# Kernel optimization log

Hardware: AMD Instinct MI355X
Metric: run time of the kernel (lower is better)

## Reference

```python
import jax, jax.numpy as jnp
import numpy as np

TEMPERATURE = 0.5

def setup_inputs() -> dict:
    key = jax.random.key(0)
    k1, k2 = jax.random.split(key)
    B, D = 4096, 256
    return {
        "first_transformed": jax.random.normal(k1, (B, D), dtype=jnp.float32),
        "second_transformed": jax.random.normal(k2, (B, D), dtype=jnp.float32),
    }

def reference(first_transformed, second_transformed):
    B = first_transformed.shape[0]
    z = jnp.concatenate([first_transformed, second_transformed], axis=0)  # [2B, D]
    z = z / jnp.linalg.norm(z, axis=1, keepdims=True)
    sim = jnp.matmul(z, z.T) / TEMPERATURE  # [2B, 2B]
    n = 2 * B
    # exclude self-similarity from the denominator (mask diagonal)
    diag_mask = jnp.eye(n, dtype=bool)
    denom = jax.nn.logsumexp(jnp.where(diag_mask, -jnp.inf, sim), axis=1)  # [2B]
    # positive pair for row i is row (i+B) mod 2B
    pos_idx = (jnp.arange(n) + B) % n
    pos = sim[jnp.arange(n), pos_idx]  # [2B]
    # loss = 1/(2B) * sum_i (-log(exp(pos_i)/denom_i)) = mean(denom - pos)
    return jnp.mean(denom - pos)
```

## Files before the change

kernel.cpp:

```cpp
#include <hip/hip_runtime.h>
#include <hip/hip_bf16.h>
#include <math.h>


#define NROWS 8192
#define BHALF 4096
#define DDIM  256
#define ROWB  512
#define JT    64
#define TILEB (JT * ROWB)
#define NSLOT 35
#define SSTRIDE 40

#define SQRT_K1 1.6986436f
#define LN2F 0.6931471805599453f

typedef __attribute__((ext_vector_type(8))) __bf16 bf16x8;
typedef __attribute__((ext_vector_type(4))) float f32x4;

#if __has_builtin(__builtin_amdgcn_exp2f)
#define FEXP2(x) __builtin_amdgcn_exp2f(x)
#else
#define FEXP2(x) __exp2f(x)
#endif
#if __has_builtin(__builtin_amdgcn_logf)
#define FLOG2(x) __builtin_amdgcn_logf(x)
#else
#define FLOG2(x) __log2f(x)
#endif

__device__ __forceinline__ float bfu(unsigned short u) {
  union { unsigned v; float f; } x; x.v = ((unsigned)u) << 16; return x.f;
}

__global__ __launch_bounds__(256) void norm_kernel(
    const float* __restrict__ a, const float* __restrict__ b,
    char* __restrict__ zb, float* __restrict__ selfdot) {
  int row = blockIdx.x * 4 + (threadIdx.x >> 6);
  int lane = threadIdx.x & 63;
  const float* src = (row < BHALF) ? (a + (size_t)row * DDIM)
                                   : (b + (size_t)(row - BHALF) * DDIM);
  float4 v = ((const float4*)src)[lane];
  float ss = v.x * v.x + v.y * v.y + v.z * v.z + v.w * v.w;
  #pragma unroll
  for (int m = 1; m < 64; m <<= 1) ss += __shfl_xor(ss, m, 64);
  float inv = rsqrtf(ss);
  inv = inv * (1.5f - 0.5f * ss * inv * inv);
  float sc = inv * SQRT_K1;

  union { __hip_bfloat16 h; unsigned short u; } c0, c1, c2, c3;
  c0.h = __float2bfloat16(v.x * sc);
  c1.h = __float2bfloat16(v.y * sc);
  c2.h = __float2bfloat16(v.z * sc);
  c3.h = __float2bfloat16(v.w * sc);
  float q0 = bfu(c0.u), q1 = bfu(c1.u), q2 = bfu(c2.u), q3 = bfu(c3.u);
  float sq = q0 * q0 + q1 * q1 + q2 * q2 + q3 * q3;
  #pragma unroll
  for (int m = 1; m < 64; m <<= 1) sq += __shfl_xor(sq, m, 64);

  ushort4 o = make_ushort4(c0.u, c1.u, c2.u, c3.u);
  int off = row * ROWB + ((lane * 8) ^ ((row & 7) << 4));
  *(ushort4*)(zb + off) = o;
  if (lane == 0) selfdot[row] = sq;
}

__global__ __launch_bounds__(256, 2) void sim_kernel(
    const char* __restrict__ zb, float* __restrict__ s_part) {
  __shared__ __align__(16) char lds[2 * TILEB];
  __shared__ float cred[2][4][64];

  int bid = blockIdx.x;
  bool heavy = (bid < 128);
  int t  = heavy ? (bid & 31) : ((bid - 128) & 31);
  int gg = heavy ? (bid >> 5) : (4 + ((bid - 128) >> 5));
  int NJT = heavy ? 5 : 4;
  int ustrip = (t + gg) & 31;
  int u16 = (t + 16) & 31;

  int wave = threadIdx.x >> 6;
  int lane = threadIdx.x & 63;
  int lrow = lane & 15;
  int kgrp = lane >> 4;
  int r0 = t * 256 + wave * 64;

  bf16x8 af[4][8];
  {
    int sw = (lrow & 7) << 4;
    #pragma unroll
    for (int rf = 0; rf < 4; ++rf) {
      const char* rp = zb + (size_t)(r0 + rf * 16 + lrow) * ROWB;
      #pragma unroll
      for (int kk = 0; kk < 8; ++kk)
        af[rf][kk] = *(const bf16x8*)(rp + ((kk * 64 + kgrp * 16) ^ sw));
    }
  }

  float sacc[4][4] = {};
  float cacc[4] = {};
  f32x4 C0, C1, C2, C3;
  bf16x8 bfv[8];

  #define STAGE_SLOT(dstbuf, j0, kkh) do {                                    \
    const char* g_ = zb +                                                     \
        (size_t)((j0) + wave * 16 + lrow) * ROWB +                            \
        (((kkh) * 64 + kgrp * 16) ^ ((lane & 7) << 4));                       \
    char* l_ = lds + (dstbuf) * TILEB + (wave * 8 + (kkh)) * 1024;            \
    __builtin_amdgcn_global_load_lds(                                         \
        (const __attribute__((address_space(1))) void*)g_,                    \
        (__attribute__((address_space(3))) void*)l_, 16, 0, 0);               \
  } while (0)

  #define DSREAD(bufi, ct) do {                                               \
    const char* lbr = lds + (bufi) * TILEB + lane * 16;                       \
    _Pragma("unroll")                                                         \
    for (int kk = 0; kk < 8; ++kk)                                            \
      bfv[kk] = *(const bf16x8*)(lbr + ((ct) * 8 + kk) * 1024);               \
  } while (0)

  #define MFMA32() do {                                                       \
    C0 = (f32x4){0.f, 0.f, 0.f, 0.f};                                         \
    C1 = (f32x4){0.f, 0.f, 0.f, 0.f};                                         \
    C2 = (f32x4){0.f, 0.f, 0.f, 0.f};                                         \
    C3 = (f32x4){0.f, 0.f, 0.f, 0.f};                                         \
    __builtin_amdgcn_s_setprio(1);                                            \
    _Pragma("unroll")                                                         \
    for (int kk = 0; kk < 8; ++kk) {                                          \
      C0 = __builtin_amdgcn_mfma_f32_16x16x32_bf16(af[0][kk], bfv[kk], C0, 0, 0, 0); \
      C1 = __builtin_amdgcn_mfma_f32_16x16x32_bf16(af[1][kk], bfv[kk], C1, 0, 0, 0); \
      C2 = __builtin_amdgcn_mfma_f32_16x16x32_bf16(af[2][kk], bfv[kk], C2, 0, 0, 0); \
      C3 = __builtin_amdgcn_mfma_f32_16x16x32_bf16(af[3][kk], bfv[kk], C3, 0, 0, 0); \
    }                                                                         \
    __builtin_amdgcn_s_setprio(0);                                            \
  } while (0)

  #define FLUSHC(ct) do {                                                     \
    float cs = 0.f;                                                           \
    _Pragma("unroll")                                                         \
    for (int r = 0; r < 4; ++r) {                                             \
      float e0 = FEXP2(C0[r]), e1 = FEXP2(C1[r]);                             \
      float e2 = FEXP2(C2[r]), e3 = FEXP2(C3[r]);                             \
      sacc[0][r] += e0; sacc[1][r] += e1;                                     \
      sacc[2][r] += e2; sacc[3][r] += e3;                                     \
      cs += (e0 + e1) + (e2 + e3);                                            \
    }                                                                         \
    cacc[ct] += cs;                                                           \
  } while (0)

  #pragma unroll
  for (int kk = 0; kk < 8; ++kk) STAGE_SLOT(0, ustrip * 256, kk);
  asm volatile("s_waitcnt vmcnt(0)" ::: "memory");
  __builtin_amdgcn_sched_barrier(0);
  __builtin_amdgcn_s_barrier();

  for (int jt = 0; jt < NJT; ++jt) {
    int nb = jt & 1;
    bool last = (jt == NJT - 1);
    int nj = jt + 1;
    int nextbase = (nj < 4) ? (ustrip * 256 + nj * 64) : (u16 * 256 + gg * 64);

    #pragma unroll
    for (int ct = 0; ct < 4; ++ct) {
      DSREAD(nb, ct);
      if (!last) {
        STAGE_SLOT(nb ^ 1, nextbase, 2 * ct);
        STAGE_SLOT(nb ^ 1, nextbase, 2 * ct + 1);
      }
      MFMA32();
      FLUSHC(ct);
    }

    bool harvest = (jt < 4) && (gg > 0);
    if (harvest) {
      #pragma unroll
      for (int c2 = 0; c2 < 4; ++c2) {
        float v = cacc[c2];
        v += __shfl_xor(v, 16, 64);
        v += __shfl_xor(v, 32, 64);
        if (kgrp == 0) cred[jt & 1][wave][c2 * 16 + lrow] = v;
      }
    }
    #pragma unroll
    for (int c2 = 0; c2 < 4; ++c2) cacc[c2] = 0.f;

    if (jt == 3 || jt == 4) {
      int slot = (jt == 3) ? gg : 16 + gg;
      #pragma unroll
      for (int rf = 0; rf < 4; ++rf) {
        #pragma unroll
        for (int r = 0; r < 4; ++r) {
          float v = sacc[rf][r];
          #pragma unroll
          for (int m = 1; m < 16; m <<= 1) v += __shfl_xor(v, m, 64);
          if (lrow == 0) {
            int grow = r0 + rf * 16 + kgrp * 4 + r;
            s_part[(size_t)grow * SSTRIDE + slot] = v;
          }
          sacc[rf][r] = 0.f;
        }
      }
    }

    asm volatile("s_waitcnt vmcnt(0)" ::: "memory");
    __builtin_amdgcn_sched_barrier(0);
    __builtin_amdgcn_s_barrier();

    if (harvest && wave == (jt & 3)) {
      int colrow = ustrip * 256 + jt * 64 + lane;
      float v = cred[jt & 1][0][lane] + cred[jt & 1][1][lane] +
                cred[jt & 1][2][lane] + cred[jt & 1][3][lane];
      s_part[(size_t)colrow * SSTRIDE + 19 + gg] = v;
    }
  }
  #undef FLUSHC
  #undef MFMA32
  #undef DSREAD
  #undef STAGE_SLOT
}

__global__ __launch_bounds__(256) void rowterm_kernel(
    const char* __restrict__ zb, const float* __restrict__ s_part,
    const float* __restrict__ selfdot, float* __restrict__ bpart) {
  int wave = threadIdx.x >> 6;
  int lane = threadIdx.x & 63;
  int rbase = blockIdx.x * 16 + wave * 4;
  float wacc = 0.f;
  #pragma unroll
  for (int rr = 0; rr < 4; ++rr) {
    int i = rbase + rr;
    int j = i ^ BHALF;
    int wo = (lane * 8) ^ ((i & 7) << 4);
    ushort4 zi = *(const ushort4*)(zb + (size_t)i * ROWB + wo);
    ushort4 zj = *(const ushort4*)(zb + (size_t)j * ROWB + wo);
    float dot = bfu(zi.x) * bfu(zj.x) + bfu(zi.y) * bfu(zj.y) +
                bfu(zi.z) * bfu(zj.z) + bfu(zi.w) * bfu(zj.w);
    float sp = (lane < NSLOT) ? s_part[(size_t)i * SSTRIDE + lane] : 0.f;
    #pragma unroll
    for (int m = 1; m < 64; m <<= 1) {
      dot += __shfl_xor(dot, m, 64);
      sp += __shfl_xor(sp, m, 64);
    }
    float S = sp - FEXP2(selfdot[i]);
    wacc += LN2F * (FLOG2(S) - dot);
  }
  __shared__ float red[4];
  if (lane == 0) red[wave] = wacc;
  __syncthreads();
  if (threadIdx.x == 0)
    bpart[blockIdx.x] = red[0] + red[1] + red[2] + red[3];
}

__global__ __launch_bounds__(512) void final_kernel(
    const float* __restrict__ bpart, float* __restrict__ out) {
  int t = threadIdx.x;
  float v = bpart[t];
  #pragma unroll
  for (int m = 1; m < 64; m <<= 1) v += __shfl_xor(v, m, 64);
  __shared__ float r2[8];
  if ((t & 63) == 0) r2[t >> 6] = v;
  __syncthreads();
  if (t == 0) {
    float s = 0.f;
    #pragma unroll
    for (int w = 0; w < 8; ++w) s += r2[w];
    out[0] = s / (float)NROWS;
  }
}

extern "C" void kernel_launch(void* const* d_in, const int* in_sizes, int n_in,
                              void* d_out, int out_size, void* d_ws, size_t ws_size,
                              hipStream_t stream) {
  const float* a = (const float*)d_in[0];
  const float* b = (const float*)d_in[1];
  float* out = (float*)d_out;
  char* ws = (char*)d_ws;

  char* zb = ws;
  float* selfdot = (float*)(ws + (size_t)NROWS * ROWB);
  float* s_part = selfdot + NROWS;
  float* bpart = s_part + (size_t)NROWS * SSTRIDE;

  hipLaunchKernelGGL(norm_kernel, dim3(NROWS / 4), dim3(256), 0, stream,
                     a, b, zb, selfdot);
  hipLaunchKernelGGL(sim_kernel, dim3(512), dim3(256), 0, stream,
                     zb, s_part);
  hipLaunchKernelGGL(rowterm_kernel, dim3(512), dim3(256), 0, stream,
                     zb, s_part, selfdot, bpart);
  hipLaunchKernelGGL(final_kernel, dim3(1), dim3(512), 0, stream, bpart, out);
}
```

Before: 43.59 us.

## Software-pipeline MFMA and exp flush with double accumulator sets

```diff
diff --git a/kernel.cpp b/kernel.cpp
--- a/kernel.cpp
+++ b/kernel.cpp
@@ -97,7 +97,8 @@
 
   float sacc[4][4] = {};
   float cacc[4] = {};
-  f32x4 C0, C1, C2, C3;
+  f32x4 X0, X1, X2, X3, Y0, Y1, Y2, Y3;
+  Y0 = Y1 = Y2 = Y3 = (f32x4){-1e30f, -1e30f, -1e30f, -1e30f};
   bf16x8 bfv[8];
 
   #define STAGE_SLOT(dstbuf, j0, kkh) do {                                    \
@@ -117,33 +118,61 @@
       bfv[kk] = *(const bf16x8*)(lbr + ((ct) * 8 + kk) * 1024);               \
   } while (0)
 
-  #define MFMA32() do {                                                       \
-    C0 = (f32x4){0.f, 0.f, 0.f, 0.f};                                         \
-    C1 = (f32x4){0.f, 0.f, 0.f, 0.f};                                         \
-    C2 = (f32x4){0.f, 0.f, 0.f, 0.f};                                         \
-    C3 = (f32x4){0.f, 0.f, 0.f, 0.f};                                         \
+  #define MFMA32(D0, D1, D2, D3) do {                                         \
+    D0 = (f32x4){0.f, 0.f, 0.f, 0.f};                                         \
+    D1 = (f32x4){0.f, 0.f, 0.f, 0.f};                                         \
+    D2 = (f32x4){0.f, 0.f, 0.f, 0.f};                                         \
+    D3 = (f32x4){0.f, 0.f, 0.f, 0.f};                                         \
     __builtin_amdgcn_s_setprio(1);                                            \
     _Pragma("unroll")                                                         \
     for (int kk = 0; kk < 8; ++kk) {                                          \
-      C0 = __builtin_amdgcn_mfma_f32_16x16x32_bf16(af[0][kk], bfv[kk], C0, 0, 0, 0); \
-      C1 = __builtin_amdgcn_mfma_f32_16x16x32_bf16(af[1][kk], bfv[kk], C1, 0, 0, 0); \
-      C2 = __builtin_amdgcn_mfma_f32_16x16x32_bf16(af[2][kk], bfv[kk], C2, 0, 0, 0); \
-      C3 = __builtin_amdgcn_mfma_f32_16x16x32_bf16(af[3][kk], bfv[kk], C3, 0, 0, 0); \
+      D0 = __builtin_amdgcn_mfma_f32_16x16x32_bf16(af[0][kk], bfv[kk], D0, 0, 0, 0); \
+      D1 = __builtin_amdgcn_mfma_f32_16x16x32_bf16(af[1][kk], bfv[kk], D1, 0, 0, 0); \
+      D2 = __builtin_amdgcn_mfma_f32_16x16x32_bf16(af[2][kk], bfv[kk], D2, 0, 0, 0); \
+      D3 = __builtin_amdgcn_mfma_f32_16x16x32_bf16(af[3][kk], bfv[kk], D3, 0, 0, 0); \
     }                                                                         \
     __builtin_amdgcn_s_setprio(0);                                            \
   } while (0)
 
-  #define FLUSHC(ct) do {                                                     \
+  #define FLUSHP(P0, P1, P2, P3, CIX) do {                                    \
     float cs = 0.f;                                                           \
     _Pragma("unroll")                                                         \
     for (int r = 0; r < 4; ++r) {                                             \
-      float e0 = FEXP2(C0[r]), e1 = FEXP2(C1[r]);                             \
-      float e2 = FEXP2(C2[r]), e3 = FEXP2(C3[r]);                             \
+      float e0 = FEXP2(P0[r]), e1 = FEXP2(P1[r]);                             \
+      float e2 = FEXP2(P2[r]), e3 = FEXP2(P3[r]);                             \
       sacc[0][r] += e0; sacc[1][r] += e1;                                     \
       sacc[2][r] += e2; sacc[3][r] += e3;                                     \
       cs += (e0 + e1) + (e2 + e3);                                            \
     }                                                                         \
-    cacc[ct] += cs;                                                           \
+    cacc[CIX] += cs;                                                          \
+  } while (0)
+
+  #define HARVEST(pj) do {                                                    \
+    _Pragma("unroll")                                                         \
+    for (int c2 = 0; c2 < 4; ++c2) {                                          \
+      float v = cacc[c2];                                                     \
+      v += __shfl_xor(v, 16, 64);                                             \
+      v += __shfl_xor(v, 32, 64);                                             \
+      if (kgrp == 0) cred[(pj) & 1][wave][c2 * 16 + lrow] = v;                \
+      cacc[c2] = 0.f;                                                         \
+    }                                                                         \
+  } while (0)
+
+  #define ROWFLUSH(slot) do {                                                 \
+    _Pragma("unroll")                                                         \
+    for (int rf = 0; rf < 4; ++rf) {                                          \
+      _Pragma("unroll")                                                       \
+      for (int r = 0; r < 4; ++r) {                                           \
+        float v = sacc[rf][r];                                                \
+        _Pragma("unroll")                                                     \
+        for (int m = 1; m < 16; m <<= 1) v += __shfl_xor(v, m, 64);           \
+        if (lrow == 0) {                                                      \
+          int grow = r0 + rf * 16 + kgrp * 4 + r;                             \
+          s_part[(size_t)grow * SSTRIDE + (slot)] = v;                        \
+        }                                                                     \
+        sacc[rf][r] = 0.f;                                                    \
+      }                                                                       \
+    }                                                                         \
   } while (0)
 
   #pragma unroll
@@ -153,65 +182,74 @@
   __builtin_amdgcn_s_barrier();
 
   for (int jt = 0; jt < NJT; ++jt) {
-    int nb = jt & 1;
+    int buf = jt & 1;
     bool last = (jt == NJT - 1);
     int nj = jt + 1;
     int nextbase = (nj < 4) ? (ustrip * 256 + nj * 64) : (u16 * 256 + gg * 64);
 
-    #pragma unroll
-    for (int ct = 0; ct < 4; ++ct) {
-      DSREAD(nb, ct);
-      if (!last) {
-        STAGE_SLOT(nb ^ 1, nextbase, 2 * ct);
-        STAGE_SLOT(nb ^ 1, nextbase, 2 * ct + 1);
-      }
-      MFMA32();
-      FLUSHC(ct);
-    }
-
-    bool harvest = (jt < 4) && (gg > 0);
-    if (harvest) {
-      #pragma unroll
-      for (int c2 = 0; c2 < 4; ++c2) {
-        float v = cacc[c2];
-        v += __shfl_xor(v, 16, 64);
-        v += __shfl_xor(v, 32, 64);
-        if (kgrp == 0) cred[jt & 1][wave][c2 * 16 + lrow] = v;
-      }
-    }
-    #pragma unroll
-    for (int c2 = 0; c2 < 4; ++c2) cacc[c2] = 0.f;
-
-    if (jt == 3 || jt == 4) {
-      int slot = (jt == 3) ? gg : 16 + gg;
-      #pragma unroll
-      for (int rf = 0; rf < 4; ++rf) {
-        #pragma unroll
-        for (int r = 0; r < 4; ++r) {
-          float v = sacc[rf][r];
-          #pragma unroll
-          for (int m = 1; m < 16; m <<= 1) v += __shfl_xor(v, m, 64);
-          if (lrow == 0) {
-            int grow = r0 + rf * 16 + kgrp * 4 + r;
-            s_part[(size_t)grow * SSTRIDE + slot] = v;
-          }
-          sacc[rf][r] = 0.f;
-        }
-      }
-    }
-
-    asm volatile("s_waitcnt vmcnt(0)" ::: "memory");
+    DSREAD(buf, 0);
+    if (!last) {
+      STAGE_SLOT(buf ^ 1, nextbase, 0);
+      STAGE_SLOT(buf ^ 1, nextbase, 1);
+      STAGE_SLOT(buf ^ 1, nextbase, 2);
+    }
+    FLUSHP(Y0, Y1, Y2, Y3, 3);
+    if (jt > 0) {
+      if (gg > 0) HARVEST(jt - 1);
+      else { cacc[0] = cacc[1] = cacc[2] = cacc[3] = 0.f; }
+      if (jt == 4) ROWFLUSH(gg);
+    }
+    MFMA32(X0, X1, X2, X3);
+    DSREAD(buf, 1);
+    if (!last) {
+      STAGE_SLOT(buf ^ 1, nextbase, 3);
+      STAGE_SLOT(buf ^ 1, nextbase, 4);
+      STAGE_SLOT(buf ^ 1, nextbase, 5);
+    }
+    FLUSHP(X0, X1, X2, X3, 0);
+    MFMA32(Y0, Y1, Y2, Y3);
+    DSREAD(buf, 2);
+    if (!last) {
+      STAGE_SLOT(buf ^ 1, nextbase, 6);
+      STAGE_SLOT(buf ^ 1, nextbase, 7);
+    }
+    FLUSHP(Y0, Y1, Y2, Y3, 1);
+    MFMA32(X0, X1, X2, X3);
+    DSREAD(buf, 3);
+    FLUSHP(X0, X1, X2, X3, 2);
+    MFMA32(Y0, Y1, Y2, Y3);
+
+    asm volatile("s_waitcnt vmcnt(0) lgkmcnt(0)" ::: "memory");
     __builtin_amdgcn_sched_barrier(0);
     __builtin_amdgcn_s_barrier();
-
-    if (harvest && wave == (jt & 3)) {
-      int colrow = ustrip * 256 + jt * 64 + lane;
-      float v = cred[jt & 1][0][lane] + cred[jt & 1][1][lane] +
-                cred[jt & 1][2][lane] + cred[jt & 1][3][lane];
+    if (jt > 0 && gg > 0 && wave == ((jt - 1) & 3)) {
+      int pj = jt - 1;
+      int colrow = ustrip * 256 + pj * 64 + lane;
+      float v = cred[pj & 1][0][lane] + cred[pj & 1][1][lane] +
+                cred[pj & 1][2][lane] + cred[pj & 1][3][lane];
       s_part[(size_t)colrow * SSTRIDE + 19 + gg] = v;
     }
   }
-  #undef FLUSHC
+
+  FLUSHP(Y0, Y1, Y2, Y3, 3);
+  if (NJT == 4) {
+    if (gg > 0) HARVEST(3);
+    ROWFLUSH(gg);
+  } else {
+    ROWFLUSH(16 + gg);
+  }
+  asm volatile("s_waitcnt lgkmcnt(0)" ::: "memory");
+  __builtin_amdgcn_sched_barrier(0);
+  __builtin_amdgcn_s_barrier();
+  if (NJT == 4 && gg > 0 && wave == 3) {
+    int colrow = ustrip * 256 + 3 * 64 + lane;
+    float v = cred[1][0][lane] + cred[1][1][lane] +
+              cred[1][2][lane] + cred[1][3][lane];
+    s_part[(size_t)colrow * SSTRIDE + 19 + gg] = v;
+  }
+  #undef ROWFLUSH
+  #undef HARVEST
+  #undef FLUSHP
   #undef MFMA32
   #undef DSREAD
   #undef STAGE_SLOT
```

New measurement: 45.86 us. 5.2% more time.

## Retile symmetric similarity into 128-row strips with uniform 3-strip-distance blocks

Applied to the files above, without the earlier changes.

```diff
diff --git a/kernel.cpp b/kernel.cpp
--- a/kernel.cpp
+++ b/kernel.cpp
@@ -7,10 +7,9 @@
 #define BHALF 4096
 #define DDIM  256
 #define ROWB  512
-#define JT    64
+#define JT    32
 #define TILEB (JT * ROWB)
-#define NSLOT 35
-#define SSTRIDE 40
+#define SSTRIDE 64
 
 #define SQRT_K1 1.6986436f
 #define LN2F 0.6931471805599453f
@@ -64,47 +63,41 @@
   if (lane == 0) selfdot[row] = sq;
 }
 
-__global__ __launch_bounds__(256, 2) void sim_kernel(
+__global__ __launch_bounds__(256, 3) void sim_kernel(
     const char* __restrict__ zb, float* __restrict__ s_part) {
   __shared__ __align__(16) char lds[2 * TILEB];
-  __shared__ float cred[2][4][64];
-
-  int bid = blockIdx.x;
-  bool heavy = (bid < 128);
-  int t  = heavy ? (bid & 31) : ((bid - 128) & 31);
-  int gg = heavy ? (bid >> 5) : (4 + ((bid - 128) >> 5));
-  int NJT = heavy ? 5 : 4;
-  int ustrip = (t + gg) & 31;
-  int u16 = (t + 16) & 31;
+  __shared__ float cred[2][4][32];
+
+  int t = blockIdx.x;
+  int b = blockIdx.y;
 
   int wave = threadIdx.x >> 6;
   int lane = threadIdx.x & 63;
   int lrow = lane & 15;
   int kgrp = lane >> 4;
-  int r0 = t * 256 + wave * 64;
-
-  bf16x8 af[4][8];
-  {
-    int sw = (lrow & 7) << 4;
-    #pragma unroll
-    for (int rf = 0; rf < 4; ++rf) {
-      const char* rp = zb + (size_t)(r0 + rf * 16 + lrow) * ROWB;
-      #pragma unroll
-      for (int kk = 0; kk < 8; ++kk)
-        af[rf][kk] = *(const bf16x8*)(rp + ((kk * 64 + kgrp * 16) ^ sw));
-    }
-  }
-
-  float sacc[4][4] = {};
-  float cacc[4] = {};
-  f32x4 C0, C1, C2, C3;
+  int sw = (lrow & 7) << 4;
+  int r0 = t * 128 + wave * 32;
+
+  bf16x8 af[2][8];
+  #pragma unroll
+  for (int rf = 0; rf < 2; ++rf) {
+    const char* rp = zb + (size_t)(r0 + rf * 16 + lrow) * ROWB;
+    #pragma unroll
+    for (int kk = 0; kk < 8; ++kk)
+      af[rf][kk] = *(const bf16x8*)(rp + ((kk * 64 + kgrp * 16) ^ sw));
+  }
+
+  float sacc[2][4] = {};
+  float cacc[2] = {};
+  f32x4 C0, C1;
   bf16x8 bfv[8];
 
-  #define STAGE_SLOT(dstbuf, j0, kkh) do {                                    \
+  #define STAGE_SLOT(dstbuf, colbase, i) do {                                 \
+    int s_ = wave * 4 + (i);                                                  \
     const char* g_ = zb +                                                     \
-        (size_t)((j0) + wave * 16 + lrow) * ROWB +                            \
-        (((kkh) * 64 + kgrp * 16) ^ ((lane & 7) << 4));                       \
-    char* l_ = lds + (dstbuf) * TILEB + (wave * 8 + (kkh)) * 1024;            \
+        (size_t)((colbase) + (s_ >> 3) * 16 + lrow) * ROWB +                  \
+        ((((s_ & 7) * 64) + kgrp * 16) ^ sw);                                 \
+    char* l_ = lds + (dstbuf) * TILEB + s_ * 1024;                            \
     __builtin_amdgcn_global_load_lds(                                         \
         (const __attribute__((address_space(1))) void*)g_,                    \
         (__attribute__((address_space(3))) void*)l_, 16, 0, 0);               \
@@ -117,18 +110,14 @@
       bfv[kk] = *(const bf16x8*)(lbr + ((ct) * 8 + kk) * 1024);               \
   } while (0)
 
-  #define MFMA32() do {                                                       \
+  #define MFMA16() do {                                                       \
     C0 = (f32x4){0.f, 0.f, 0.f, 0.f};                                         \
     C1 = (f32x4){0.f, 0.f, 0.f, 0.f};                                         \
-    C2 = (f32x4){0.f, 0.f, 0.f, 0.f};                                         \
-    C3 = (f32x4){0.f, 0.f, 0.f, 0.f};                                         \
     __builtin_amdgcn_s_setprio(1);                                            \
     _Pragma("unroll")                                                         \
     for (int kk = 0; kk < 8; ++kk) {                                          \
       C0 = __builtin_amdgcn_mfma_f32_16x16x32_bf16(af[0][kk], bfv[kk], C0, 0, 0, 0); \
       C1 = __builtin_amdgcn_mfma_f32_16x16x32_bf16(af[1][kk], bfv[kk], C1, 0, 0, 0); \
-      C2 = __builtin_amdgcn_mfma_f32_16x16x32_bf16(af[2][kk], bfv[kk], C2, 0, 0, 0); \
-      C3 = __builtin_amdgcn_mfma_f32_16x16x32_bf16(af[3][kk], bfv[kk], C3, 0, 0, 0); \
     }                                                                         \
     __builtin_amdgcn_s_setprio(0);                                            \
   } while (0)
@@ -138,54 +127,60 @@
     _Pragma("unroll")                                                         \
     for (int r = 0; r < 4; ++r) {                                             \
       float e0 = FEXP2(C0[r]), e1 = FEXP2(C1[r]);                             \
-      float e2 = FEXP2(C2[r]), e3 = FEXP2(C3[r]);                             \
       sacc[0][r] += e0; sacc[1][r] += e1;                                     \
-      sacc[2][r] += e2; sacc[3][r] += e3;                                     \
-      cs += (e0 + e1) + (e2 + e3);                                            \
+      cs += e0 + e1;                                                          \
     }                                                                         \
     cacc[ct] += cs;                                                           \
   } while (0)
 
-  #pragma unroll
-  for (int kk = 0; kk < 8; ++kk) STAGE_SLOT(0, ustrip * 256, kk);
+  #define COLBASE(q) ((((t + 3 * b + ((q) >> 2)) & 63) << 7) + (((q) & 3) << 5))
+
+  {
+    int cb0 = COLBASE(0);
+    #pragma unroll
+    for (int i = 0; i < 4; ++i) STAGE_SLOT(0, cb0, i);
+  }
   asm volatile("s_waitcnt vmcnt(0)" ::: "memory");
   __builtin_amdgcn_sched_barrier(0);
   __builtin_amdgcn_s_barrier();
 
-  for (int jt = 0; jt < NJT; ++jt) {
-    int nb = jt & 1;
-    bool last = (jt == NJT - 1);
-    int nj = jt + 1;
-    int nextbase = (nj < 4) ? (ustrip * 256 + nj * 64) : (u16 * 256 + gg * 64);
-
-    #pragma unroll
-    for (int ct = 0; ct < 4; ++ct) {
-      DSREAD(nb, ct);
-      if (!last) {
-        STAGE_SLOT(nb ^ 1, nextbase, 2 * ct);
-        STAGE_SLOT(nb ^ 1, nextbase, 2 * ct + 1);
-      }
-      MFMA32();
-      FLUSHC(ct);
-    }
-
-    bool harvest = (jt < 4) && (gg > 0);
+  for (int jt = 0; jt < 12; ++jt) {
+    int buf = jt & 1;
+    int d = 3 * b + (jt >> 2);
+    int u = (t + d) & 63;
+    bool last = (jt == 11);
+    int nextbase = last ? 0 : COLBASE(jt + 1);
+
+    DSREAD(buf, 0);
+    if (!last) {
+      STAGE_SLOT(buf ^ 1, nextbase, 0);
+      STAGE_SLOT(buf ^ 1, nextbase, 1);
+    }
+    MFMA16();
+    FLUSHC(0);
+    DSREAD(buf, 1);
+    if (!last) {
+      STAGE_SLOT(buf ^ 1, nextbase, 2);
+      STAGE_SLOT(buf ^ 1, nextbase, 3);
+    }
+    MFMA16();
+    FLUSHC(1);
+
+    bool harvest = (d >= 1) && (d <= 31);
     if (harvest) {
       #pragma unroll
-      for (int c2 = 0; c2 < 4; ++c2) {
+      for (int c2 = 0; c2 < 2; ++c2) {
         float v = cacc[c2];
         v += __shfl_xor(v, 16, 64);
         v += __shfl_xor(v, 32, 64);
         if (kgrp == 0) cred[jt & 1][wave][c2 * 16 + lrow] = v;
       }
     }
-    #pragma unroll
-    for (int c2 = 0; c2 < 4; ++c2) cacc[c2] = 0.f;
-
-    if (jt == 3 || jt == 4) {
-      int slot = (jt == 3) ? gg : 16 + gg;
+    cacc[0] = 0.f; cacc[1] = 0.f;
+
+    if ((jt & 3) == 3) {
       #pragma unroll
-      for (int rf = 0; rf < 4; ++rf) {
+      for (int rf = 0; rf < 2; ++rf) {
         #pragma unroll
         for (int r = 0; r < 4; ++r) {
           float v = sacc[rf][r];
@@ -193,26 +188,27 @@
           for (int m = 1; m < 16; m <<= 1) v += __shfl_xor(v, m, 64);
           if (lrow == 0) {
             int grow = r0 + rf * 16 + kgrp * 4 + r;
-            s_part[(size_t)grow * SSTRIDE + slot] = v;
+            s_part[(size_t)grow * SSTRIDE + d] = v;
           }
           sacc[rf][r] = 0.f;
         }
       }
     }
 
-    asm volatile("s_waitcnt vmcnt(0)" ::: "memory");
+    asm volatile("s_waitcnt vmcnt(0) lgkmcnt(0)" ::: "memory");
     __builtin_amdgcn_sched_barrier(0);
     __builtin_amdgcn_s_barrier();
 
-    if (harvest && wave == (jt & 3)) {
-      int colrow = ustrip * 256 + jt * 64 + lane;
+    if (harvest && wave == (jt & 3) && lane < 32) {
+      int colrow = u * 128 + (jt & 3) * 32 + lane;
       float v = cred[jt & 1][0][lane] + cred[jt & 1][1][lane] +
                 cred[jt & 1][2][lane] + cred[jt & 1][3][lane];
-      s_part[(size_t)colrow * SSTRIDE + 19 + gg] = v;
-    }
-  }
+      s_part[(size_t)colrow * SSTRIDE + 32 + d] = v;
+    }
+  }
+  #undef COLBASE
   #undef FLUSHC
-  #undef MFMA32
+  #undef MFMA16
   #undef DSREAD
   #undef STAGE_SLOT
 }
@@ -233,7 +229,7 @@
     ushort4 zj = *(const ushort4*)(zb + (size_t)j * ROWB + wo);
     float dot = bfu(zi.x) * bfu(zj.x) + bfu(zi.y) * bfu(zj.y) +
                 bfu(zi.z) * bfu(zj.z) + bfu(zi.w) * bfu(zj.w);
-    float sp = (lane < NSLOT) ? s_part[(size_t)i * SSTRIDE + lane] : 0.f;
+    float sp = s_part[(size_t)i * SSTRIDE + lane];
     #pragma unroll
     for (int m = 1; m < 64; m <<= 1) {
       dot += __shfl_xor(dot, m, 64);
@@ -281,7 +277,7 @@
 
   hipLaunchKernelGGL(norm_kernel, dim3(NROWS / 4), dim3(256), 0, stream,
                      a, b, zb, selfdot);
-  hipLaunchKernelGGL(sim_kernel, dim3(512), dim3(256), 0, stream,
+  hipLaunchKernelGGL(sim_kernel, dim3(64, 11), dim3(256), 0, stream,
                      zb, s_part);
   hipLaunchKernelGGL(rowterm_kernel, dim3(512), dim3(256), 0, stream,
                      zb, s_part, selfdot, bpart);
```

After: 42.10 us, median of 3. 1.04x faster.
